# Optimization experiments

Measured on AMD Instinct MI355X. Metric: run time of the kernel, lower is better.

Reference implementation:

```python
import jax, jax.numpy as jnp
import numpy as np

N_NODES = 50000
N_EDGES = 800000
D = 64           # node feature / hidden dim for all 5 GCN layers
NUM_GRAPHS = 512
FINAL_NEURON = 128
OUT_DIM = 1
NUM_LAYERS = 5


def setup_inputs() -> dict:
    key = jax.random.key(0)
    ks = jax.random.split(key, 20)
    inp = {}
    inp["x"] = jax.random.normal(ks[0], (N_NODES, D), dtype=jnp.float32)
    inp["edge_index"] = jax.random.randint(ks[1], (2, N_EDGES), 0, N_NODES)
    inp["batch"] = jnp.sort(jax.random.randint(ks[2], (N_NODES,), 0, NUM_GRAPHS))
    # GCNConv weights (Glorot-ish) and biases for 5 layers, all D->D
    for i in range(NUM_LAYERS):
        inp[f"W{i+1}"] = jax.random.normal(ks[3 + i], (D, D), dtype=jnp.float32) / np.sqrt(D)
        inp[f"b{i+1}"] = jnp.zeros((D,), dtype=jnp.float32)
    inp["fc1_W"] = jax.random.normal(ks[10], (D, FINAL_NEURON), dtype=jnp.float32) / np.sqrt(D)
    inp["fc1_b"] = jnp.zeros((FINAL_NEURON,), dtype=jnp.float32)
    inp["fc2_W"] = jax.random.normal(ks[11], (FINAL_NEURON, OUT_DIM), dtype=jnp.float32) / np.sqrt(FINAL_NEURON)
    inp["fc2_b"] = jnp.zeros((OUT_DIM,), dtype=jnp.float32)
    return inp


def _gcn_conv(h, src, dst, dinv, W, b):
    # PyG GCNConv: x' = D^{-1/2} (A + I) D^{-1/2} (h W) + b, deg includes self-loop
    hw = h @ W                                           # [N, D_out]
    norm_e = dinv[src] * dinv[dst]                       # [E]
    msg = hw[src] * norm_e[:, None]                      # gather + scale
    agg = jax.ops.segment_sum(msg, dst, num_segments=h.shape[0])
    agg = agg + (dinv * dinv)[:, None] * hw              # self-loop contribution
    return agg + b


def reference(x, edge_index, batch, W1, b1, W2, b2, W3, b3, W4, b4, W5, b5,
              fc1_W, fc1_b, fc2_W, fc2_b):
    src, dst = edge_index[0], edge_index[1]
    n = x.shape[0]
    # degree on A + I (in-degree at dst, plus 1 self-loop)
    deg = jax.ops.segment_sum(jnp.ones(src.shape[0], x.dtype), dst, num_segments=n) + 1.0
    dinv = jax.lax.rsqrt(deg)
    h = x
    for W, b in ((W1, b1), (W2, b2), (W3, b3), (W4, b4), (W5, b5)):
        h = jax.nn.relu(_gcn_conv(h, src, dst, dinv, W, b))
    # global_add_pool readout over graph ids
    g = jax.ops.segment_sum(h, batch, num_segments=NUM_GRAPHS)   # [G, D]
    g = jax.nn.relu(g @ fc1_W + fc1_b)
    return g @ fc2_W + fc2_b                                     # [G, 1]
```

## Files before the change

kernel.cpp:

```cpp
#include <hip/hip_runtime.h>
#include <hip/hip_fp16.h>

#define N_NODES 50000
#define N_EDGES 800000
#define D 64
#define NUM_GRAPHS 512
#define FINAL_NEURON 128
#define SCAN_NB ((N_NODES + 255) / 256)

#define BN 16
#define NB_GEMM (N_NODES / BN)
#define NB_EDGE (N_EDGES / 256)
#define ZS 72
#define WS 72
#define WELEM (D * WS)

typedef unsigned short ushort_t;
typedef _Float16 f16;
typedef __attribute__((ext_vector_type(4))) _Float16 f16x4;
typedef __attribute__((ext_vector_type(8))) _Float16 f16x8;
typedef __attribute__((ext_vector_type(4))) float f32x4;

struct WPtrs { const float* w[5]; };

__device__ __forceinline__ float2 h2f(unsigned v) {
    __half2 h = *reinterpret_cast<__half2*>(&v);
    return __half22float2(h);
}

__device__ __forceinline__ void acc_add8(float4& a0, float4& a1, uint4 u) {
    float2 p;
    p = h2f(u.x); a0.x += p.x; a0.y += p.y;
    p = h2f(u.y); a0.z += p.x; a0.w += p.y;
    p = h2f(u.z); a1.x += p.x; a1.y += p.y;
    p = h2f(u.w); a1.z += p.x; a1.w += p.y;
}

__global__ void k_zero_prep(int* cnt, WPtrs wp, f16* __restrict__ whi, f16* __restrict__ wlo) {
    int b = blockIdx.x;
    if (b < SCAN_NB) {
        int i = b * 256 + threadIdx.x;
        if (i < N_NODES) cnt[i] = 0;
        return;
    }
    int l = b - SCAN_NB;
    const float* W = wp.w[l];
    f16* hi = whi + l * WELEM;
    f16* lo = wlo + l * WELEM;
    for (int idx = threadIdx.x; idx < D * D; idx += 256) {
        int k = idx >> 6, j = idx & 63;
        float w = W[idx];
        f16 h = (f16)w;
        hi[j * WS + k] = h;
        lo[j * WS + k] = (f16)(w - (float)h);
    }
}

__global__ void k_hist(const int* __restrict__ dst, int* cnt, ushort_t* __restrict__ epos) {
    int e = blockIdx.x * blockDim.x + threadIdx.x;
    if (e < N_EDGES) epos[e] = (ushort_t)atomicAdd(&cnt[dst[e]], 1);
}

__global__ void k_blocksum(const int* __restrict__ cnt, int* __restrict__ bsum,
                           float* __restrict__ dinv, float* __restrict__ g) {
    __shared__ int sdata[256];
    int t = threadIdx.x;
    int i = blockIdx.x * 256 + t;
    int v = (i < N_NODES) ? cnt[i] : 0;
    if (i < N_NODES) dinv[i] = rsqrtf((float)v + 1.0f);
    if (i < NUM_GRAPHS * D) g[i] = 0.f;
    sdata[t] = v;
    __syncthreads();
    for (int s = 128; s > 0; s >>= 1) {
        if (t < s) sdata[t] += sdata[t + s];
        __syncthreads();
    }
    if (t == 0) bsum[blockIdx.x] = sdata[0];
}

__global__ void k_scanbsum(const int* __restrict__ bsum, int* __restrict__ boff) {
    __shared__ int buf[256];
    int t = threadIdx.x;
    int v = (t < SCAN_NB) ? bsum[t] : 0;
    buf[t] = v;
    __syncthreads();
    for (int off = 1; off < 256; off <<= 1) {
        int a = (t >= off) ? buf[t - off] : 0;
        __syncthreads();
        buf[t] += a;
        __syncthreads();
    }
    if (t < SCAN_NB) boff[t] = buf[t] - v;
}

__global__ void k_localscan(const int* __restrict__ cnt, const int* __restrict__ boff,
                            int* __restrict__ row) {
    __shared__ int buf[256];
    int t = threadIdx.x;
    int i = blockIdx.x * 256 + t;
    int v = (i < N_NODES) ? cnt[i] : 0;
    buf[t] = v;
    __syncthreads();
    for (int off = 1; off < 256; off <<= 1) {
        int a = (t >= off) ? buf[t - off] : 0;
        __syncthreads();
        buf[t] += a;
        __syncthreads();
    }
    if (i < N_NODES) row[i] = boff[blockIdx.x] + buf[t] - v;
    if (i == 0) row[N_NODES] = N_EDGES;
}

__device__ __forceinline__ void gather_half(const int* __restrict__ row,
                                            const ushort_t* __restrict__ esrc,
                                            const uint4* __restrict__ hp,
                                            int n, int g, int q,
                                            float4& a0, float4& a1) {
    int e0 = row[n], e1 = row[n + 1];
    int len = e1 - e0;
    int h0 = (len + 1) >> 1;
    int e  = g ? (e0 + h0) : e0;
    int eg = g ? e1 : (e0 + h0);
    if (g) acc_add8(a0, a1, hp[(size_t)n * 8 + q]);
    int m = eg - e;
    int i0, i1, i2, i3, i4, i5, i6, i7;
    if (m >= 8) {
        i0 = esrc[e];     i1 = esrc[e + 1]; i2 = esrc[e + 2]; i3 = esrc[e + 3];
        i4 = esrc[e + 4]; i5 = esrc[e + 5]; i6 = esrc[e + 6]; i7 = esrc[e + 7];
        for (;;) {
            uint4 u0 = hp[(size_t)i0 * 8 + q], u1 = hp[(size_t)i1 * 8 + q];
            uint4 u2 = hp[(size_t)i2 * 8 + q], u3 = hp[(size_t)i3 * 8 + q];
            uint4 u4 = hp[(size_t)i4 * 8 + q], u5 = hp[(size_t)i5 * 8 + q];
            uint4 u6 = hp[(size_t)i6 * 8 + q], u7 = hp[(size_t)i7 * 8 + q];
            e += 8; m -= 8;
            i0 = esrc[e];     i1 = esrc[e + 1]; i2 = esrc[e + 2]; i3 = esrc[e + 3];
            i4 = esrc[e + 4]; i5 = esrc[e + 5]; i6 = esrc[e + 6]; i7 = esrc[e + 7];
            acc_add8(a0, a1, u0); acc_add8(a0, a1, u1);
            acc_add8(a0, a1, u2); acc_add8(a0, a1, u3);
            acc_add8(a0, a1, u4); acc_add8(a0, a1, u5);
            acc_add8(a0, a1, u6); acc_add8(a0, a1, u7);
            if (m < 8) break;
        }
    } else {
        if (m <= 0) return;
        i0 = esrc[e];     i1 = esrc[e + 1]; i2 = esrc[e + 2]; i3 = esrc[e + 3];
        i4 = esrc[e + 4]; i5 = esrc[e + 5]; i6 = esrc[e + 6]; i7 = esrc[e + 7];
    }
    if (m & 4) {
        uint4 u0 = hp[(size_t)i0 * 8 + q], u1 = hp[(size_t)i1 * 8 + q];
        uint4 u2 = hp[(size_t)i2 * 8 + q], u3 = hp[(size_t)i3 * 8 + q];
        acc_add8(a0, a1, u0); acc_add8(a0, a1, u1);
        acc_add8(a0, a1, u2); acc_add8(a0, a1, u3);
        i0 = i4; i1 = i5; i2 = i6; i3 = i7;
    }
    if (m & 2) {
        uint4 u0 = hp[(size_t)i0 * 8 + q], u1 = hp[(size_t)i1 * 8 + q];
        acc_add8(a0, a1, u0); acc_add8(a0, a1, u1);
        i0 = i2; i1 = i3;
    }
    if (m & 1) {
        uint4 u0 = hp[(size_t)i0 * 8 + q];
        acc_add8(a0, a1, u0);
    }
}

__device__ __forceinline__ void gemm_16x64_reg(f16* zsh,
                                               const f16* __restrict__ whi_g,
                                               const f16* __restrict__ wlo_g,
                                               const float* dinvsh, int t) {
    int w = t >> 6, l = t & 63;
    int cb = w * 16;
    int lr = l & 15, lg = l >> 4;
    const f16* bhp = &whi_g[(cb + lr) * WS + lg * 8];
    const f16* blp = &wlo_g[(cb + lr) * WS + lg * 8];
    f16x8 bh0 = *(const f16x8*)bhp;
    f16x8 bl0 = *(const f16x8*)blp;
    f16x8 bh1 = *(const f16x8*)(bhp + 32);
    f16x8 bl1 = *(const f16x8*)(blp + 32);
    f32x4 acc = {0.f, 0.f, 0.f, 0.f};
    f16x8 a0 = *(const f16x8*)&zsh[lr * ZS + lg * 8];
    f16x8 a1 = *(const f16x8*)&zsh[lr * ZS + 32 + lg * 8];
    acc = __builtin_amdgcn_mfma_f32_16x16x32_f16(a0, bh0, acc, 0, 0, 0);
    acc = __builtin_amdgcn_mfma_f32_16x16x32_f16(a0, bl0, acc, 0, 0, 0);
    acc = __builtin_amdgcn_mfma_f32_16x16x32_f16(a1, bh1, acc, 0, 0, 0);
    acc = __builtin_amdgcn_mfma_f32_16x16x32_f16(a1, bl1, acc, 0, 0, 0);
    __syncthreads();
#pragma unroll
    for (int r = 0; r < 4; ++r) {
        int rrow = lg * 4 + r;
        float s = dinvsh[rrow];
        zsh[rrow * ZS + cb + lr] = (f16)(acc[r] * s);
    }
}

__global__ __launch_bounds__(256, 8)
void k_transform0(const float* __restrict__ x, const float* __restrict__ dinv,
                  const f16* __restrict__ whi_g, const f16* __restrict__ wlo_g,
                  __half* __restrict__ hout,
                  const int* __restrict__ src, const int* __restrict__ dst,
                  const int* __restrict__ row, const ushort_t* __restrict__ epos,
                  ushort_t* __restrict__ esrc) {
    int t = threadIdx.x;
    if (blockIdx.x >= NB_GEMM) {
        int e = (blockIdx.x - NB_GEMM) * 256 + t;
        if (e < N_EDGES) esrc[row[dst[e]] + (int)epos[e]] = (ushort_t)src[e];
        return;
    }
    __shared__ __attribute__((aligned(16))) f16 zsh[BN * ZS];
    __shared__ float dinvsh[BN];
    int base = blockIdx.x * BN;
    if (t < BN) dinvsh[t] = dinv[base + t];

    int nl = t >> 4, c4 = t & 15;
    float4 xv = ((const float4*)x)[(size_t)(base + nl) * 16 + c4];
    f16x4 zv = {(f16)xv.x, (f16)xv.y, (f16)xv.z, (f16)xv.w};
    *(f16x4*)&zsh[nl * ZS + c4 * 4] = zv;
    __syncthreads();
    gemm_16x64_reg(zsh, whi_g, wlo_g, dinvsh, t);
    __syncthreads();
    if (t < 128) {
        int n2 = t >> 3, q = t & 7;
        uint4 o = *(const uint4*)&zsh[n2 * ZS + q * 8];
        ((uint4*)hout)[(size_t)(base + n2) * 8 + q] = o;
    }
}

__global__ __launch_bounds__(256, 7)
void k_layer(const int* __restrict__ row, const ushort_t* __restrict__ esrc,
             const __half* __restrict__ hin, const float* __restrict__ dinv,
             const float* __restrict__ bias,
             const f16* __restrict__ whi_g, const f16* __restrict__ wlo_g,
             __half* __restrict__ hout) {
    __shared__ __attribute__((aligned(16))) f16 zsh[BN * ZS];
    __shared__ float dinvsh[BN];
    int t = threadIdx.x;
    int base = blockIdx.x * BN;
    if (t < BN) dinvsh[t] = dinv[base + t];

    int nl = t >> 4, m = t & 15, g = m >> 3, q = m & 7;
    int n = base + nl;
    float4 a0 = {0,0,0,0}, a1 = {0,0,0,0};
    gather_half(row, esrc, (const uint4*)hin, n, g, q, a0, a1);
    a0.x += __shfl_xor(a0.x, 8); a0.y += __shfl_xor(a0.y, 8);
    a0.z += __shfl_xor(a0.z, 8); a0.w += __shfl_xor(a0.w, 8);
    a1.x += __shfl_xor(a1.x, 8); a1.y += __shfl_xor(a1.y, 8);
    a1.z += __shfl_xor(a1.z, 8); a1.w += __shfl_xor(a1.w, 8);
    float s = dinv[n];
    float4 b0 = ((const float4*)bias)[2 * q];
    float4 b1 = ((const float4*)bias)[2 * q + 1];
    if (g == 0) {
        f16x8 zv;
        zv[0] = (f16)fmaxf(a0.x * s + b0.x, 0.f);
        zv[1] = (f16)fmaxf(a0.y * s + b0.y, 0.f);
        zv[2] = (f16)fmaxf(a0.z * s + b0.z, 0.f);
        zv[3] = (f16)fmaxf(a0.w * s + b0.w, 0.f);
        zv[4] = (f16)fmaxf(a1.x * s + b1.x, 0.f);
        zv[5] = (f16)fmaxf(a1.y * s + b1.y, 0.f);
        zv[6] = (f16)fmaxf(a1.z * s + b1.z, 0.f);
        zv[7] = (f16)fmaxf(a1.w * s + b1.w, 0.f);
        *(f16x8*)&zsh[nl * ZS + q * 8] = zv;
    }
    __syncthreads();
    gemm_16x64_reg(zsh, whi_g, wlo_g, dinvsh, t);
    __syncthreads();
    if (t < 128) {
        int n2 = t >> 3, q2 = t & 7;
        uint4 o = *(const uint4*)&zsh[n2 * ZS + q2 * 8];
        ((uint4*)hout)[(size_t)(base + n2) * 8 + q2] = o;
    }
}

__global__ __launch_bounds__(256, 7)
void k_layer_pool(const int* __restrict__ row, const ushort_t* __restrict__ esrc,
                  const __half* __restrict__ hin, const float* __restrict__ dinv,
                  const float* __restrict__ bias, const int* __restrict__ batch,
                  float* __restrict__ g) {
    __shared__ float zf[BN * 68];
    __shared__ int bsh[BN];
    int t = threadIdx.x;
    int base = blockIdx.x * BN;
    if (t < BN) bsh[t] = batch[base + t];

    int nl = t >> 4, m = t & 15, g2 = m >> 3, q = m & 7;
    int n = base + nl;
    float4 a0 = {0,0,0,0}, a1 = {0,0,0,0};
    gather_half(row, esrc, (const uint4*)hin, n, g2, q, a0, a1);
    a0.x += __shfl_xor(a0.x, 8); a0.y += __shfl_xor(a0.y, 8);
    a0.z += __shfl_xor(a0.z, 8); a0.w += __shfl_xor(a0.w, 8);
    a1.x += __shfl_xor(a1.x, 8); a1.y += __shfl_xor(a1.y, 8);
    a1.z += __shfl_xor(a1.z, 8); a1.w += __shfl_xor(a1.w, 8);
    float s = dinv[n];
    float4 b0 = ((const float4*)bias)[2 * q];
    float4 b1 = ((const float4*)bias)[2 * q + 1];
    if (g2 == 0) {
        float4 r0, r1;
        r0.x = fmaxf(a0.x * s + b0.x, 0.f);
        r0.y = fmaxf(a0.y * s + b0.y, 0.f);
        r0.z = fmaxf(a0.z * s + b0.z, 0.f);
        r0.w = fmaxf(a0.w * s + b0.w, 0.f);
        r1.x = fmaxf(a1.x * s + b1.x, 0.f);
        r1.y = fmaxf(a1.y * s + b1.y, 0.f);
        r1.z = fmaxf(a1.z * s + b1.z, 0.f);
        r1.w = fmaxf(a1.w * s + b1.w, 0.f);
        *(float4*)&zf[nl * 68 + q * 8]     = r0;
        *(float4*)&zf[nl * 68 + q * 8 + 4] = r1;
    }
    __syncthreads();
    int f = t & 63, grp = t >> 6;
    int n0 = grp * 4;
    int cur = bsh[n0];
    float acc = 0.f;
#pragma unroll
    for (int k2 = 0; k2 < 4; ++k2) {
        int bb = bsh[n0 + k2];
        if (bb != cur) { atomicAdd(&g[cur * D + f], acc); acc = 0.f; cur = bb; }
        acc += zf[(n0 + k2) * 68 + f];
    }
    atomicAdd(&g[cur * D + f], acc);
}

__global__ void k_mlp(const float* __restrict__ g, const float* __restrict__ W1,
                      const float* __restrict__ b1, const float* __restrict__ W2,
                      const float* __restrict__ b2, float* __restrict__ out) {
    __shared__ float red[FINAL_NEURON];
    int row = blockIdx.x;
    int j = threadIdx.x;
    float acc = 0.f;
#pragma unroll
    for (int k = 0; k < D; ++k) acc += g[row * D + k] * W1[k * FINAL_NEURON + j];
    acc = fmaxf(acc + b1[j], 0.f);
    red[j] = acc * W2[j];
    __syncthreads();
    for (int s = 64; s > 0; s >>= 1) {
        if (j < s) red[j] += red[j + s];
        __syncthreads();
    }
    if (j == 0) out[row] = red[0] + b2[0];
}

extern "C" void kernel_launch(void* const* d_in, const int* in_sizes, int n_in,
                              void* d_out, int out_size, void* d_ws, size_t ws_size,
                              hipStream_t stream) {
    const float* x     = (const float*)d_in[0];
    const int*   ei    = (const int*)d_in[1];
    const int*   src   = ei;
    const int*   dst   = ei + N_EDGES;
    const int*   batch = (const int*)d_in[2];
    WPtrs wp;
    wp.w[0] = (const float*)d_in[3];  wp.w[1] = (const float*)d_in[5];
    wp.w[2] = (const float*)d_in[7];  wp.w[3] = (const float*)d_in[9];
    wp.w[4] = (const float*)d_in[11];
    const float* b[5]  = {(const float*)d_in[4], (const float*)d_in[6], (const float*)d_in[8],
                          (const float*)d_in[10], (const float*)d_in[12]};
    const float* fc1W  = (const float*)d_in[13];
    const float* fc1b  = (const float*)d_in[14];
    const float* fc2W  = (const float*)d_in[15];
    const float* fc2b  = (const float*)d_in[16];
    float* out = (float*)d_out;

    __half*   yA   = (__half*)d_ws;
    __half*   yB   = yA + (size_t)N_NODES * D;
    f16*      whiG = (f16*)(yB + (size_t)N_NODES * D);
    f16*      wloG = whiG + 5 * WELEM;
    float*    g    = (float*)(wloG + 5 * WELEM);
    float*    dinv = g + NUM_GRAPHS * D;
    int*      cnt  = (int*)(dinv + N_NODES);
    int*      row  = cnt + N_NODES;
    int*      bsum = row + N_NODES + 1;
    int*      boff = bsum + 256;
    ushort_t* epos = (ushort_t*)(boff + 256);
    ushort_t* esrc = epos + N_EDGES;

    k_zero_prep<<<SCAN_NB + 5, 256, 0, stream>>>(cnt, wp, whiG, wloG);
    k_hist<<<(N_EDGES + 255) / 256, 256, 0, stream>>>(dst, cnt, epos);
    k_blocksum<<<SCAN_NB, 256, 0, stream>>>(cnt, bsum, dinv, g);
    k_scanbsum<<<1, 256, 0, stream>>>(bsum, boff);
    k_localscan<<<SCAN_NB, 256, 0, stream>>>(cnt, boff, row);

    k_transform0<<<NB_GEMM + NB_EDGE, 256, 0, stream>>>(x, dinv, whiG, wloG, yA,
                                                        src, dst, row, epos, esrc);

    k_layer<<<NB_GEMM, 256, 0, stream>>>(row, esrc, yA, dinv, b[0],
                                         whiG + 1 * WELEM, wloG + 1 * WELEM, yB);
    k_layer<<<NB_GEMM, 256, 0, stream>>>(row, esrc, yB, dinv, b[1],
                                         whiG + 2 * WELEM, wloG + 2 * WELEM, yA);
    k_layer<<<NB_GEMM, 256, 0, stream>>>(row, esrc, yA, dinv, b[2],
                                         whiG + 3 * WELEM, wloG + 3 * WELEM, yB);
    k_layer<<<NB_GEMM, 256, 0, stream>>>(row, esrc, yB, dinv, b[3],
                                         whiG + 4 * WELEM, wloG + 4 * WELEM, yA);

    k_layer_pool<<<NB_GEMM, 256, 0, stream>>>(row, esrc, yA, dinv, b[4], batch, g);

    k_mlp<<<NUM_GRAPHS, FINAL_NEURON, 0, stream>>>(g, fc1W, fc1b, fc2W, fc2b, out);
}
```

Measured before the change: 242.6 us.

## Process two node tiles per layer block with prefetched edge indices; atomic CSR fill

Each k_layer block now handles two 16-node tiles and prefetches the second tile's CSR row bounds and first eight source indices while the first tile's gather runs, halving the grid and hiding index-load latency. Separately, the CSR build drops the per-edge epos array: the histogram no longer records positions, and the scatter pass takes its slot with an atomicAdd on a per-node cursor. The atomic fill makes neighbor order within a row nondeterministic, which changes the float summation order. Fewer blocks also lowers parallelism, and the second tile runs serially after the first GEMM.

Measured after the change: 298.7 us. 1.23x slower.

```diff
diff --git a/kernel.cpp b/kernel.cpp
--- a/kernel.cpp
+++ b/kernel.cpp
@@ -10,6 +10,7 @@
 
 #define BN 16
 #define NB_GEMM (N_NODES / BN)
+#define NBL ((NB_GEMM + 1) / 2)
 #define NB_EDGE (N_EDGES / 256)
 #define ZS 72
 #define WS 72
@@ -56,9 +57,9 @@
     }
 }
 
-__global__ void k_hist(const int* __restrict__ dst, int* cnt, ushort_t* __restrict__ epos) {
+__global__ void k_hist(const int* __restrict__ dst, int* cnt) {
     int e = blockIdx.x * blockDim.x + threadIdx.x;
-    if (e < N_EDGES) epos[e] = (ushort_t)atomicAdd(&cnt[dst[e]], 1);
+    if (e < N_EDGES) atomicAdd(&cnt[dst[e]], 1);
 }
 
 __global__ void k_blocksum(const int* __restrict__ cnt, int* __restrict__ bsum,
@@ -94,7 +95,7 @@
 }
 
 __global__ void k_localscan(const int* __restrict__ cnt, const int* __restrict__ boff,
-                            int* __restrict__ row) {
+                            int* __restrict__ row, int* __restrict__ cur) {
     __shared__ int buf[256];
     int t = threadIdx.x;
     int i = blockIdx.x * 256 + t;
@@ -107,26 +108,37 @@
         buf[t] += a;
         __syncthreads();
     }
-    if (i < N_NODES) row[i] = boff[blockIdx.x] + buf[t] - v;
+    if (i < N_NODES) {
+        int r = boff[blockIdx.x] + buf[t] - v;
+        row[i] = r;
+        cur[i] = r;
+    }
     if (i == 0) row[N_NODES] = N_EDGES;
 }
 
-__device__ __forceinline__ void gather_half(const int* __restrict__ row,
+struct GS { int e, m; int i0, i1, i2, i3, i4, i5, i6, i7; };
+
+__device__ __forceinline__ void gh_prologue(const int* __restrict__ row,
                                             const ushort_t* __restrict__ esrc,
-                                            const uint4* __restrict__ hp,
-                                            int n, int g, int q,
-                                            float4& a0, float4& a1) {
+                                            int n, int g, GS& S) {
     int e0 = row[n], e1 = row[n + 1];
-    int len = e1 - e0;
-    int h0 = (len + 1) >> 1;
+    int h0 = (e1 - e0 + 1) >> 1;
     int e  = g ? (e0 + h0) : e0;
     int eg = g ? e1 : (e0 + h0);
+    S.e = e; S.m = eg - e;
+    S.i0 = esrc[e];     S.i1 = esrc[e + 1]; S.i2 = esrc[e + 2]; S.i3 = esrc[e + 3];
+    S.i4 = esrc[e + 4]; S.i5 = esrc[e + 5]; S.i6 = esrc[e + 6]; S.i7 = esrc[e + 7];
+}
+
+__device__ __forceinline__ void gh_rounds(const ushort_t* __restrict__ esrc,
+                                          const uint4* __restrict__ hp,
+                                          int n, int g, int q, GS S,
+                                          float4& a0, float4& a1) {
     if (g) acc_add8(a0, a1, hp[(size_t)n * 8 + q]);
-    int m = eg - e;
-    int i0, i1, i2, i3, i4, i5, i6, i7;
+    int e = S.e, m = S.m;
+    int i0 = S.i0, i1 = S.i1, i2 = S.i2, i3 = S.i3;
+    int i4 = S.i4, i5 = S.i5, i6 = S.i6, i7 = S.i7;
     if (m >= 8) {
-        i0 = esrc[e];     i1 = esrc[e + 1]; i2 = esrc[e + 2]; i3 = esrc[e + 3];
-        i4 = esrc[e + 4]; i5 = esrc[e + 5]; i6 = esrc[e + 6]; i7 = esrc[e + 7];
         for (;;) {
             uint4 u0 = hp[(size_t)i0 * 8 + q], u1 = hp[(size_t)i1 * 8 + q];
             uint4 u2 = hp[(size_t)i2 * 8 + q], u3 = hp[(size_t)i3 * 8 + q];
@@ -141,11 +153,8 @@
             acc_add8(a0, a1, u6); acc_add8(a0, a1, u7);
             if (m < 8) break;
         }
-    } else {
-        if (m <= 0) return;
-        i0 = esrc[e];     i1 = esrc[e + 1]; i2 = esrc[e + 2]; i3 = esrc[e + 3];
-        i4 = esrc[e + 4]; i5 = esrc[e + 5]; i6 = esrc[e + 6]; i7 = esrc[e + 7];
-    }
+    }
+    if (m <= 0) return;
     if (m & 4) {
         uint4 u0 = hp[(size_t)i0 * 8 + q], u1 = hp[(size_t)i1 * 8 + q];
         uint4 u2 = hp[(size_t)i2 * 8 + q], u3 = hp[(size_t)i3 * 8 + q];
@@ -198,12 +207,14 @@
                   const f16* __restrict__ whi_g, const f16* __restrict__ wlo_g,
                   __half* __restrict__ hout,
                   const int* __restrict__ src, const int* __restrict__ dst,
-                  const int* __restrict__ row, const ushort_t* __restrict__ epos,
-                  ushort_t* __restrict__ esrc) {
+                  int* __restrict__ cur, ushort_t* __restrict__ esrc) {
     int t = threadIdx.x;
     if (blockIdx.x >= NB_GEMM) {
         int e = (blockIdx.x - NB_GEMM) * 256 + t;
-        if (e < N_EDGES) esrc[row[dst[e]] + (int)epos[e]] = (ushort_t)src[e];
+        if (e < N_EDGES) {
+            int slot = atomicAdd(&cur[dst[e]], 1);
+            esrc[slot] = (ushort_t)src[e];
+        }
         return;
     }
     __shared__ __attribute__((aligned(16))) f16 zsh[BN * ZS];
@@ -232,41 +243,86 @@
              const f16* __restrict__ whi_g, const f16* __restrict__ wlo_g,
              __half* __restrict__ hout) {
     __shared__ __attribute__((aligned(16))) f16 zsh[BN * ZS];
-    __shared__ float dinvsh[BN];
-    int t = threadIdx.x;
-    int base = blockIdx.x * BN;
-    if (t < BN) dinvsh[t] = dinv[base + t];
-
-    int nl = t >> 4, m = t & 15, g = m >> 3, q = m & 7;
-    int n = base + nl;
-    float4 a0 = {0,0,0,0}, a1 = {0,0,0,0};
-    gather_half(row, esrc, (const uint4*)hin, n, g, q, a0, a1);
+    __shared__ float dinvsh[2][BN];
+    int t = threadIdx.x;
+    int tile0 = blockIdx.x * 2;
+    int base0 = tile0 * BN;
+    int base1 = base0 + BN;
+    bool has1 = (tile0 + 1 < NB_GEMM);
+    if (t < BN) {
+        dinvsh[0][t] = dinv[base0 + t];
+        if (has1) dinvsh[1][t] = dinv[base1 + t];
+    }
+    int nl = t >> 4, m16 = t & 15, g = m16 >> 3, q = m16 & 7;
+    float4 bb0 = ((const float4*)bias)[2 * q];
+    float4 bb1 = ((const float4*)bias)[2 * q + 1];
+    const uint4* hp = (const uint4*)hin;
+
+    GS S;
+    gh_prologue(row, esrc, base0 + nl, g, S);
+    float4 a0, a1;
+    a0.x = a0.y = a0.z = a0.w = 0.f;
+    a1.x = a1.y = a1.z = a1.w = 0.f;
+    gh_rounds(esrc, hp, base0 + nl, g, q, S, a0, a1);
+    GS SB;
+    if (has1) gh_prologue(row, esrc, base1 + nl, g, SB);
+
     a0.x += __shfl_xor(a0.x, 8); a0.y += __shfl_xor(a0.y, 8);
     a0.z += __shfl_xor(a0.z, 8); a0.w += __shfl_xor(a0.w, 8);
     a1.x += __shfl_xor(a1.x, 8); a1.y += __shfl_xor(a1.y, 8);
     a1.z += __shfl_xor(a1.z, 8); a1.w += __shfl_xor(a1.w, 8);
-    float s = dinv[n];
-    float4 b0 = ((const float4*)bias)[2 * q];
-    float4 b1 = ((const float4*)bias)[2 * q + 1];
     if (g == 0) {
+        float s = dinvsh[0][nl];
         f16x8 zv;
-        zv[0] = (f16)fmaxf(a0.x * s + b0.x, 0.f);
-        zv[1] = (f16)fmaxf(a0.y * s + b0.y, 0.f);
-        zv[2] = (f16)fmaxf(a0.z * s + b0.z, 0.f);
-        zv[3] = (f16)fmaxf(a0.w * s + b0.w, 0.f);
-        zv[4] = (f16)fmaxf(a1.x * s + b1.x, 0.f);
-        zv[5] = (f16)fmaxf(a1.y * s + b1.y, 0.f);
-        zv[6] = (f16)fmaxf(a1.z * s + b1.z, 0.f);
-        zv[7] = (f16)fmaxf(a1.w * s + b1.w, 0.f);
+        zv[0] = (f16)fmaxf(a0.x * s + bb0.x, 0.f);
+        zv[1] = (f16)fmaxf(a0.y * s + bb0.y, 0.f);
+        zv[2] = (f16)fmaxf(a0.z * s + bb0.z, 0.f);
+        zv[3] = (f16)fmaxf(a0.w * s + bb0.w, 0.f);
+        zv[4] = (f16)fmaxf(a1.x * s + bb1.x, 0.f);
+        zv[5] = (f16)fmaxf(a1.y * s + bb1.y, 0.f);
+        zv[6] = (f16)fmaxf(a1.z * s + bb1.z, 0.f);
+        zv[7] = (f16)fmaxf(a1.w * s + bb1.w, 0.f);
         *(f16x8*)&zsh[nl * ZS + q * 8] = zv;
     }
     __syncthreads();
-    gemm_16x64_reg(zsh, whi_g, wlo_g, dinvsh, t);
+    gemm_16x64_reg(zsh, whi_g, wlo_g, dinvsh[0], t);
     __syncthreads();
     if (t < 128) {
         int n2 = t >> 3, q2 = t & 7;
         uint4 o = *(const uint4*)&zsh[n2 * ZS + q2 * 8];
-        ((uint4*)hout)[(size_t)(base + n2) * 8 + q2] = o;
+        ((uint4*)hout)[(size_t)(base0 + n2) * 8 + q2] = o;
+    }
+
+    if (has1) {
+        __syncthreads();
+        a0.x = a0.y = a0.z = a0.w = 0.f;
+        a1.x = a1.y = a1.z = a1.w = 0.f;
+        gh_rounds(esrc, hp, base1 + nl, g, q, SB, a0, a1);
+        a0.x += __shfl_xor(a0.x, 8); a0.y += __shfl_xor(a0.y, 8);
+        a0.z += __shfl_xor(a0.z, 8); a0.w += __shfl_xor(a0.w, 8);
+        a1.x += __shfl_xor(a1.x, 8); a1.y += __shfl_xor(a1.y, 8);
+        a1.z += __shfl_xor(a1.z, 8); a1.w += __shfl_xor(a1.w, 8);
+        if (g == 0) {
+            float s = dinvsh[1][nl];
+            f16x8 zv;
+            zv[0] = (f16)fmaxf(a0.x * s + bb0.x, 0.f);
+            zv[1] = (f16)fmaxf(a0.y * s + bb0.y, 0.f);
+            zv[2] = (f16)fmaxf(a0.z * s + bb0.z, 0.f);
+            zv[3] = (f16)fmaxf(a0.w * s + bb0.w, 0.f);
+            zv[4] = (f16)fmaxf(a1.x * s + bb1.x, 0.f);
+            zv[5] = (f16)fmaxf(a1.y * s + bb1.y, 0.f);
+            zv[6] = (f16)fmaxf(a1.z * s + bb1.z, 0.f);
+            zv[7] = (f16)fmaxf(a1.w * s + bb1.w, 0.f);
+            *(f16x8*)&zsh[nl * ZS + q * 8] = zv;
+        }
+        __syncthreads();
+        gemm_16x64_reg(zsh, whi_g, wlo_g, dinvsh[1], t);
+        __syncthreads();
+        if (t < 128) {
+            int n2 = t >> 3, q2 = t & 7;
+            uint4 o = *(const uint4*)&zsh[n2 * ZS + q2 * 8];
+            ((uint4*)hout)[(size_t)(base1 + n2) * 8 + q2] = o;
+        }
     }
 }
 
@@ -283,8 +339,12 @@
 
     int nl = t >> 4, m = t & 15, g2 = m >> 3, q = m & 7;
     int n = base + nl;
-    float4 a0 = {0,0,0,0}, a1 = {0,0,0,0};
-    gather_half(row, esrc, (const uint4*)hin, n, g2, q, a0, a1);
+    GS S;
+    gh_prologue(row, esrc, n, g2, S);
+    float4 a0, a1;
+    a0.x = a0.y = a0.z = a0.w = 0.f;
+    a1.x = a1.y = a1.z = a1.w = 0.f;
+    gh_rounds(esrc, (const uint4*)hin, n, g2, q, S, a0, a1);
     a0.x += __shfl_xor(a0.x, 8); a0.y += __shfl_xor(a0.y, 8);
     a0.z += __shfl_xor(a0.z, 8); a0.w += __shfl_xor(a0.w, 8);
     a1.x += __shfl_xor(a1.x, 8); a1.y += __shfl_xor(a1.y, 8);
@@ -366,28 +426,28 @@
     float*    dinv = g + NUM_GRAPHS * D;
     int*      cnt  = (int*)(dinv + N_NODES);
     int*      row  = cnt + N_NODES;
-    int*      bsum = row + N_NODES + 1;
+    int*      cur  = row + N_NODES + 1;
+    int*      bsum = cur + N_NODES;
     int*      boff = bsum + 256;
-    ushort_t* epos = (ushort_t*)(boff + 256);
-    ushort_t* esrc = epos + N_EDGES;
+    ushort_t* esrc = (ushort_t*)(boff + 256);
 
     k_zero_prep<<<SCAN_NB + 5, 256, 0, stream>>>(cnt, wp, whiG, wloG);
-    k_hist<<<(N_EDGES + 255) / 256, 256, 0, stream>>>(dst, cnt, epos);
+    k_hist<<<(N_EDGES + 255) / 256, 256, 0, stream>>>(dst, cnt);
     k_blocksum<<<SCAN_NB, 256, 0, stream>>>(cnt, bsum, dinv, g);
     k_scanbsum<<<1, 256, 0, stream>>>(bsum, boff);
-    k_localscan<<<SCAN_NB, 256, 0, stream>>>(cnt, boff, row);
+    k_localscan<<<SCAN_NB, 256, 0, stream>>>(cnt, boff, row, cur);
 
     k_transform0<<<NB_GEMM + NB_EDGE, 256, 0, stream>>>(x, dinv, whiG, wloG, yA,
-                                                        src, dst, row, epos, esrc);
-
-    k_layer<<<NB_GEMM, 256, 0, stream>>>(row, esrc, yA, dinv, b[0],
-                                         whiG + 1 * WELEM, wloG + 1 * WELEM, yB);
-    k_layer<<<NB_GEMM, 256, 0, stream>>>(row, esrc, yB, dinv, b[1],
-                                         whiG + 2 * WELEM, wloG + 2 * WELEM, yA);
-    k_layer<<<NB_GEMM, 256, 0, stream>>>(row, esrc, yA, dinv, b[2],
-                                         whiG + 3 * WELEM, wloG + 3 * WELEM, yB);
-    k_layer<<<NB_GEMM, 256, 0, stream>>>(row, esrc, yB, dinv, b[3],
-                                         whiG + 4 * WELEM, wloG + 4 * WELEM, yA);
+                                                        src, dst, cur, esrc);
+
+    k_layer<<<NBL, 256, 0, stream>>>(row, esrc, yA, dinv, b[0],
+                                     whiG + 1 * WELEM, wloG + 1 * WELEM, yB);
+    k_layer<<<NBL, 256, 0, stream>>>(row, esrc, yB, dinv, b[1],
+                                     whiG + 2 * WELEM, wloG + 2 * WELEM, yA);
+    k_layer<<<NBL, 256, 0, stream>>>(row, esrc, yA, dinv, b[2],
+                                     whiG + 3 * WELEM, wloG + 3 * WELEM, yB);
+    k_layer<<<NBL, 256, 0, stream>>>(row, esrc, yB, dinv, b[3],
+                                     whiG + 4 * WELEM, wloG + 4 * WELEM, yA);
 
     k_layer_pool<<<NB_GEMM, 256, 0, stream>>>(row, esrc, yA, dinv, b[4], batch, g);
 
```
